# Kernel tuning notes

Measured on AMD Instinct MI355X. Metric: run time of the kernel, lower is better.

## Reference

```python
import jax, jax.numpy as jnp
import numpy as np

N = 100000      # nodes
E = 1600000     # edges (before self-loops)
F_IN = 128      # num_features
H = 4           # heads
C = 32          # out_channels per head (num_hidden)
SLOPE = 0.2     # leaky relu negative slope (alpha)


def setup_inputs() -> dict:
    key = jax.random.key(0)
    k = jax.random.split(key, 6)
    x = jax.random.normal(k[0], (N, F_IN), jnp.float32)
    edge_index = jax.random.randint(k[1], (2, E), 0, N, dtype=jnp.int64)
    W = jax.random.normal(k[2], (F_IN, H * C), jnp.float32) * (1.0 / np.sqrt(F_IN))
    att_src = jax.random.normal(k[3], (H, C), jnp.float32) * 0.1
    att_dst = jax.random.normal(k[4], (H, C), jnp.float32) * 0.1
    bias = jnp.zeros((H * C,), jnp.float32)
    return dict(x=x, W=W, att_src=att_src, att_dst=att_dst, bias=bias,
                edge_index=edge_index)


def reference(x, W, att_src, att_dst, bias, edge_index):
    # PyG GATConv (concat=True, add_self_loops=True), eval mode (dropout off).
    loops = jnp.arange(N, dtype=edge_index.dtype)
    ei = jnp.concatenate([edge_index, jnp.stack([loops, loops])], axis=1)
    src, dst = ei[0], ei[1]                     # [E+N]

    h = (x @ W).reshape(N, H, C)                # projected node features
    a_src = jnp.einsum('nhc,hc->nh', h, att_src)   # [N, H]
    a_dst = jnp.einsum('nhc,hc->nh', h, att_dst)   # [N, H]

    e = a_src[src] + a_dst[dst]                 # [E+N, H]
    e = jnp.where(e > 0, e, SLOPE * e)          # leaky relu

    # segment softmax over incoming edges of each dst node (per head)
    m = jax.lax.stop_gradient(jax.ops.segment_max(e, dst, num_segments=N))
    p = jnp.exp(e - m[dst])
    denom = jax.ops.segment_sum(p, dst, num_segments=N)
    alpha = p / (denom[dst] + 1e-16)            # [E+N, H]

    # weighted scatter-aggregate of source features
    out = jax.ops.segment_sum(alpha[:, :, None] * h[src], dst, num_segments=N)
    return out.reshape(N, H * C) + bias
```

## Files before the change

### kernel.cpp

```cpp
#include <hip/hip_runtime.h>
#include <hip/hip_bf16.h>
#include <math.h>

#define N_NODES 100000
#define F_IN    128
#define HC      128
#define NH      4
#define SLOPE   0.2f

#define PADK    136

#define NB      196
#define BSH     9
#define CAP     10240
#define CAPC    10752
#define CHUNK   2048
#define CURPAD  16

#define GEMM_BLOCKS 1563

typedef __attribute__((ext_vector_type(8))) short short8;
typedef __attribute__((ext_vector_type(4))) float f32x4;
typedef __attribute__((ext_vector_type(2))) float fx2;

static __device__ __forceinline__ float leaky(float x) { return x > 0.f ? x : SLOPE * x; }

static __device__ __forceinline__ short f2bs(float f) {
    __hip_bfloat16 b = __float2bfloat16(f);
    return *reinterpret_cast<short*>(&b);
}

__global__ __launch_bounds__(256) void k_pre(const float* __restrict__ W,
                                             unsigned short* __restrict__ wt,
                                             int* __restrict__ bucket_cursor)
{
    int t = blockIdx.x * 256 + threadIdx.x;
    if (t < 128 * 128) {
        int k = t >> 7, n = t & 127;
        wt[n * 128 + k] = (unsigned short)f2bs(W[k * HC + n]);
    }
    if (t < NB * CURPAD) bucket_cursor[t] = 0;
}

union SMem {
    struct {
        short xs[64 * PADK];
        short ws[128 * PADK];
    } g;
    struct {
        int ebuf[CHUNK];
        unsigned char bkt[CHUNK];
        int hist[256];
        int lexcl[257];
        int gbase[256];
        int sdata[256];
    } b;
};

__global__ __launch_bounds__(256) void k_main(const float* __restrict__ x,
                                              const unsigned short* __restrict__ wt,
                                              const float* __restrict__ att_src,
                                              const float* __restrict__ att_dst,
                                              unsigned short* __restrict__ hb,
                                              float* __restrict__ a_src,
                                              float* __restrict__ a_dst,
                                              const int* __restrict__ srcp,
                                              const int* __restrict__ dstp,
                                              int* __restrict__ bucket_cursor,
                                              int* __restrict__ eb, int E)
{
    __shared__ SMem sm;
    const int t = threadIdx.x;

    if (blockIdx.x < GEMM_BLOCKS) {
        const int r0 = blockIdx.x * 64;

        for (int i = t; i < 2048; i += 256) {
            int row = i >> 5, kq = (i & 31) * 4;
            int gr = r0 + row;
            float4 v = make_float4(0.f, 0.f, 0.f, 0.f);
            if (gr < N_NODES) v = ((const float4*)(x + (size_t)gr * F_IN))[i & 31];
            short* p = &sm.g.xs[row * PADK + kq];
            p[0] = f2bs(v.x); p[1] = f2bs(v.y); p[2] = f2bs(v.z); p[3] = f2bs(v.w);
        }
        for (int i = t; i < 2048; i += 256) {
            int n = i >> 4, k0 = (i & 15) * 8;
            *(float4*)&sm.g.ws[n * PADK + k0] = *(const float4*)&wt[n * 128 + k0];
        }
        __syncthreads();

        const int wave = t >> 6, lane = t & 63;
        const int quad = lane >> 4, l16 = lane & 15;
        const int wrow = wave * 16;

        f32x4 acc[8];
        #pragma unroll
        for (int nt = 0; nt < 8; ++nt) acc[nt] = (f32x4){0.f, 0.f, 0.f, 0.f};

        const short* ap = &sm.g.xs[(wrow + l16) * PADK + quad * 8];
        #pragma unroll
        for (int kb = 0; kb < 4; ++kb) {
            short8 a = *(const short8*)(ap + kb * 32);
            #pragma unroll
            for (int nt = 0; nt < 8; ++nt) {
                short8 b = *(const short8*)&sm.g.ws[(nt * 16 + l16) * PADK + kb * 32 + quad * 8];
                acc[nt] = __builtin_amdgcn_mfma_f32_16x16x32_bf16(a, b, acc[nt], 0, 0, 0);
            }
        }

        float att_s[8], att_d[8];
        #pragma unroll
        for (int nt = 0; nt < 8; ++nt) {
            att_s[nt] = att_src[nt * 16 + l16];
            att_d[nt] = att_dst[nt * 16 + l16];
        }

        #pragma unroll
        for (int g = 0; g < 4; ++g) {
            int r = r0 + wrow + quad * 4 + g;
            if (r < N_NODES) {
                #pragma unroll
                for (int nt = 0; nt < 8; ++nt)
                    hb[(size_t)r * HC + nt * 16 + l16] = (unsigned short)f2bs(acc[nt][g]);
            }
            float s0 = acc[0][g] * att_s[0] + acc[1][g] * att_s[1];
            float s1 = acc[2][g] * att_s[2] + acc[3][g] * att_s[3];
            float s2 = acc[4][g] * att_s[4] + acc[5][g] * att_s[5];
            float s3 = acc[6][g] * att_s[6] + acc[7][g] * att_s[7];
            float d0 = acc[0][g] * att_d[0] + acc[1][g] * att_d[1];
            float d1 = acc[2][g] * att_d[2] + acc[3][g] * att_d[3];
            float d2 = acc[4][g] * att_d[4] + acc[5][g] * att_d[5];
            float d3 = acc[6][g] * att_d[6] + acc[7][g] * att_d[7];
            #pragma unroll
            for (int o = 1; o < 16; o <<= 1) {
                s0 += __shfl_xor(s0, o); s1 += __shfl_xor(s1, o);
                s2 += __shfl_xor(s2, o); s3 += __shfl_xor(s3, o);
                d0 += __shfl_xor(d0, o); d1 += __shfl_xor(d1, o);
                d2 += __shfl_xor(d2, o); d3 += __shfl_xor(d3, o);
            }
            if (l16 == 0 && r < N_NODES) {
                *(float4*)&a_src[r * NH] = make_float4(s0, s1, s2, s3);
                *(float4*)&a_dst[r * NH] = make_float4(d0, d1, d2, d3);
            }
        }
    } else {
        const int base = (blockIdx.x - GEMM_BLOCKS) * CHUNK;

        sm.b.hist[t] = 0;
        __syncthreads();

        #pragma unroll
        for (int j = 0; j < CHUNK / 256; ++j) {
            int i = base + t + j * 256;
            if (i < E) atomicAdd(&sm.b.hist[dstp[i] >> BSH], 1);
        }
        __syncthreads();

        int cnt = sm.b.hist[t];
        sm.b.sdata[t] = cnt;
        __syncthreads();
        for (int o = 1; o < 256; o <<= 1) {
            int add = (t >= o) ? sm.b.sdata[t - o] : 0;
            __syncthreads();
            sm.b.sdata[t] += add;
            __syncthreads();
        }
        int excl = sm.b.sdata[t] - cnt;
        sm.b.lexcl[t] = excl;
        if (t == 255) sm.b.lexcl[256] = sm.b.sdata[255];
        sm.b.hist[t] = excl;
        int gb = 0;
        if (t < NB && cnt > 0) gb = atomicAdd(&bucket_cursor[t * CURPAD], cnt);
        sm.b.gbase[t] = t * CAP + gb;
        __syncthreads();

        #pragma unroll
        for (int j = 0; j < CHUNK / 256; ++j) {
            int i = base + t + j * 256;
            if (i < E) {
                int s = srcp[i], d = dstp[i];
                int b = d >> BSH;
                int r = atomicAdd(&sm.b.hist[b], 1);
                sm.b.ebuf[r] = (s << BSH) | (d & 511);
                sm.b.bkt[r] = (unsigned char)b;
            }
        }
        __syncthreads();

        const int blockTotal = sm.b.lexcl[256];
        for (int i = t; i < blockTotal; i += 256) {
            int b = sm.b.bkt[i];
            eb[sm.b.gbase[b] + (i - sm.b.lexcl[b])] = sm.b.ebuf[i];
        }
    }
}

__global__ __launch_bounds__(1024) void k_csr(const int* __restrict__ eb,
                                              const int* __restrict__ bucket_cursor,
                                              int* __restrict__ col,
                                              int2* __restrict__ rowse)
{
    __shared__ int deg[512];
    __shared__ int sdata[256];

    const int t  = threadIdx.x;
    const int b  = blockIdx.x;
    const int n0 = b * 512;
    const int cnt   = bucket_cursor[b * CURPAD];
    const int ebase = b * CAP;
    const int gofs  = b * CAPC;

    if (t < 512) deg[t] = (n0 + t < N_NODES) ? 1 : 0;
    __syncthreads();

    for (int i = t; i < cnt; i += 1024)
        atomicAdd(&deg[eb[ebase + i] & 511], 1);
    __syncthreads();

    int d0 = 0, d1 = 0, ps = 0;
    if (t < 256) {
        d0 = deg[2 * t]; d1 = deg[2 * t + 1];
        ps = d0 + d1;
        sdata[t] = ps;
    }
    __syncthreads();
    for (int o = 1; o < 256; o <<= 1) {
        int add = 0;
        if (t < 256 && t >= o) add = sdata[t - o];
        __syncthreads();
        if (t < 256) sdata[t] += add;
        __syncthreads();
    }
    if (t < 256) {
        int e0 = sdata[t] - ps;
        int e1 = e0 + d0;
        int na = n0 + 2 * t, nb2 = n0 + 2 * t + 1;
        if (na < N_NODES) {
            rowse[na] = make_int2(gofs + e0, gofs + e0 + d0);
            col[gofs + e0] = na;
        }
        if (nb2 < N_NODES) {
            rowse[nb2] = make_int2(gofs + e1, gofs + e1 + d1);
            col[gofs + e1] = nb2;
        }
        deg[2 * t]     = e0 + 1;
        deg[2 * t + 1] = e1 + 1;
    }
    __syncthreads();

    for (int i = t; i < cnt; i += 1024) {
        int v = eb[ebase + i];
        int r = atomicAdd(&deg[v & 511], 1);
        col[gofs + r] = v >> BSH;
    }
}

__global__ __launch_bounds__(256) void k_node(const unsigned short* __restrict__ hb,
                                              const float* __restrict__ a_src,
                                              const float* __restrict__ a_dst,
                                              const int2* __restrict__ rowse,
                                              const int* __restrict__ col,
                                              const float* __restrict__ bias,
                                              float* __restrict__ out)
{
    const int lane = threadIdx.x & 63;
    const int node = blockIdx.x * 4 + (threadIdx.x >> 6);
    if (node >= N_NODES) return;

    const int2 se = rowse[node];
    const int r0 = se.x, r1 = se.y;
    const int myh = lane >> 4;
    const float adm = a_dst[node * NH + myh];

    float denom = 0.f, acc0 = 0.f, acc1 = 0.f;
    int i = r0;
    for (; i + 8 <= r1; i += 8) {
        int s[8];
        #pragma unroll
        for (int j = 0; j < 8; ++j) s[j] = col[i + j];
        float as[8];
        #pragma unroll
        for (int j = 0; j < 8; ++j) as[j] = a_src[s[j] * NH + myh];
        unsigned int hv[8];
        #pragma unroll
        for (int j = 0; j < 8; ++j)
            hv[j] = *(const unsigned int*)&hb[(size_t)s[j] * HC + 2 * lane];
        #pragma unroll
        for (int j = 0; j < 8; ++j) {
            float p = __expf(leaky(as[j] + adm));
            denom += p;
            acc0 += p * __uint_as_float(hv[j] << 16);
            acc1 += p * __uint_as_float(hv[j] & 0xffff0000u);
        }
    }
    for (; i < r1; ++i) {
        int s = col[i];
        float p = __expf(leaky(a_src[s * NH + myh] + adm));
        unsigned int v = *(const unsigned int*)&hb[(size_t)s * HC + 2 * lane];
        denom += p;
        acc0 += p * __uint_as_float(v << 16);
        acc1 += p * __uint_as_float(v & 0xffff0000u);
    }

    float inv = 1.f / (denom + 1e-16f);
    fx2 o2;
    o2.x = acc0 * inv + bias[2 * lane];
    o2.y = acc1 * inv + bias[2 * lane + 1];
    __builtin_nontemporal_store(o2, (fx2*)&out[(size_t)node * HC + 2 * lane]);
}

extern "C" void kernel_launch(void* const* d_in, const int* in_sizes, int n_in,
                              void* d_out, int out_size, void* d_ws, size_t ws_size,
                              hipStream_t stream)
{
    const float* x       = (const float*)d_in[0];
    const float* W       = (const float*)d_in[1];
    const float* att_src = (const float*)d_in[2];
    const float* att_dst = (const float*)d_in[3];
    const float* bias    = (const float*)d_in[4];
    const int*   ei      = (const int*)d_in[5];
    const int E = in_sizes[5] / 2;
    const int* srcp = ei;
    const int* dstp = ei + E;
    float* out = (float*)d_out;

    char* wsb = (char*)d_ws;
    size_t off = 0;
    auto alloc = [&](size_t bytes) -> char* {
        char* p = wsb + off;
        off += (bytes + 255) & ~(size_t)255;
        return p;
    };
    unsigned short* hb = (unsigned short*)alloc((size_t)N_NODES * HC * sizeof(unsigned short));
    float* a_src   = (float*)alloc((size_t)N_NODES * NH * sizeof(float));
    float* a_dst   = (float*)alloc((size_t)N_NODES * NH * sizeof(float));
    int*   eb      = (int*)alloc((size_t)NB * CAP * sizeof(int));
    int*   col     = (int*)alloc((size_t)NB * CAPC * sizeof(int));
    int2*  rowse   = (int2*)alloc((size_t)N_NODES * sizeof(int2));
    int*   bcursor = (int*)alloc((size_t)NB * CURPAD * sizeof(int));
    unsigned short* wt = (unsigned short*)alloc(128 * 128 * sizeof(unsigned short));

    const int bucketBlocks = (E + CHUNK - 1) / CHUNK;

    k_pre<<<64, 256, 0, stream>>>(W, wt, bcursor);
    k_main<<<GEMM_BLOCKS + bucketBlocks, 256, 0, stream>>>(x, wt, att_src, att_dst,
                                                           hb, a_src, a_dst,
                                                           srcp, dstp, bcursor, eb, E);
    k_csr<<<NB, 1024, 0, stream>>>(eb, bcursor, col, rowse);
    k_node<<<(N_NODES + 3) / 4, 256, 0, stream>>>(hb, a_src, a_dst, rowse, col, bias, out);
}
```

Before: 251.0 us.

## Move bucketing to own kernel, fuse CSR build with GEMM, widen node gather

Edge bucketing now runs in its own kernel. The CSR construction (256-thread blocks) is merged into the same launch as the projection GEMM, so the CSR work overlaps with the dense compute and one launch goes away. The per-node aggregation is also restructured: each wave handles four edges at once with 16-byte feature loads per lane, then reduces across lane groups with shuffles before the store. The cost is an extra shuffle reduction, and the CSR part runs with fewer threads per bucket.

Result: no change. 247.4 us (-1.4%).

```diff
diff --git a/kernel.cpp b/kernel.cpp
--- a/kernel.cpp
+++ b/kernel.cpp
@@ -17,11 +17,8 @@
 #define CHUNK   2048
 #define CURPAD  16
 
-#define GEMM_BLOCKS 1563
-
 typedef __attribute__((ext_vector_type(8))) short short8;
 typedef __attribute__((ext_vector_type(4))) float f32x4;
-typedef __attribute__((ext_vector_type(2))) float fx2;
 
 static __device__ __forceinline__ float leaky(float x) { return x > 0.f ? x : SLOPE * x; }
 
@@ -40,6 +37,69 @@
         wt[n * 128 + k] = (unsigned short)f2bs(W[k * HC + n]);
     }
     if (t < NB * CURPAD) bucket_cursor[t] = 0;
+}
+
+__global__ __launch_bounds__(256) void k_bucket(const int* __restrict__ srcp,
+                                                const int* __restrict__ dstp,
+                                                int* __restrict__ bucket_cursor,
+                                                int* __restrict__ eb, int E)
+{
+    __shared__ int ebuf[CHUNK];
+    __shared__ unsigned char bkt[CHUNK];
+    __shared__ int hist[256];
+    __shared__ int lexcl[257];
+    __shared__ int gbase[256];
+    __shared__ int sdata[256];
+
+    const int t = threadIdx.x;
+    const int base = blockIdx.x * CHUNK;
+
+    hist[t] = 0;
+    __syncthreads();
+
+    #pragma unroll
+    for (int j = 0; j < CHUNK / 256; ++j) {
+        int i = base + t + j * 256;
+        if (i < E) atomicAdd(&hist[dstp[i] >> BSH], 1);
+    }
+    __syncthreads();
+
+    int cnt = hist[t];
+    sdata[t] = cnt;
+    __syncthreads();
+    for (int o = 1; o < 256; o <<= 1) {
+        int add = (t >= o) ? sdata[t - o] : 0;
+        __syncthreads();
+        sdata[t] += add;
+        __syncthreads();
+    }
+    int excl = sdata[t] - cnt;
+    lexcl[t] = excl;
+    if (t == 255) lexcl[256] = sdata[255];
+    hist[t] = excl;
+    int gb = 0;
+    if (t < NB && cnt > 0) gb = atomicAdd(&bucket_cursor[t * CURPAD], cnt);
+    gbase[t] = t * CAP + gb;
+    __syncthreads();
+
+    #pragma unroll
+    for (int j = 0; j < CHUNK / 256; ++j) {
+        int i = base + t + j * 256;
+        if (i < E) {
+            int s = srcp[i], d = dstp[i];
+            int b = d >> BSH;
+            int r = atomicAdd(&hist[b], 1);
+            ebuf[r] = (s << BSH) | (d & 511);
+            bkt[r] = (unsigned char)b;
+        }
+    }
+    __syncthreads();
+
+    const int blockTotal = lexcl[256];
+    for (int i = t; i < blockTotal; i += 256) {
+        int b = bkt[i];
+        eb[gbase[b] + (i - lexcl[b])] = ebuf[i];
+    }
 }
 
 union SMem {
@@ -48,32 +108,75 @@
         short ws[128 * PADK];
     } g;
     struct {
-        int ebuf[CHUNK];
-        unsigned char bkt[CHUNK];
-        int hist[256];
-        int lexcl[257];
-        int gbase[256];
+        int deg[512];
         int sdata[256];
-    } b;
+    } c;
 };
 
-__global__ __launch_bounds__(256) void k_main(const float* __restrict__ x,
-                                              const unsigned short* __restrict__ wt,
-                                              const float* __restrict__ att_src,
-                                              const float* __restrict__ att_dst,
-                                              unsigned short* __restrict__ hb,
-                                              float* __restrict__ a_src,
-                                              float* __restrict__ a_dst,
-                                              const int* __restrict__ srcp,
-                                              const int* __restrict__ dstp,
-                                              int* __restrict__ bucket_cursor,
-                                              int* __restrict__ eb, int E)
+__global__ __launch_bounds__(256) void k_fused(const float* __restrict__ x,
+                                               const unsigned short* __restrict__ wt,
+                                               const float* __restrict__ att_src,
+                                               const float* __restrict__ att_dst,
+                                               unsigned short* __restrict__ hb,
+                                               float* __restrict__ a_src,
+                                               float* __restrict__ a_dst,
+                                               const int* __restrict__ eb,
+                                               const int* __restrict__ bucket_cursor,
+                                               int* __restrict__ col,
+                                               int2* __restrict__ rowse)
 {
     __shared__ SMem sm;
     const int t = threadIdx.x;
 
-    if (blockIdx.x < GEMM_BLOCKS) {
-        const int r0 = blockIdx.x * 64;
+    if (blockIdx.x < NB) {
+        const int b  = blockIdx.x;
+        const int n0 = b * 512;
+        const int cnt   = bucket_cursor[b * CURPAD];
+        const int ebase = b * CAP;
+        const int gofs  = b * CAPC;
+
+        sm.c.deg[t]       = (n0 + t       < N_NODES) ? 1 : 0;
+        sm.c.deg[t + 256] = (n0 + t + 256 < N_NODES) ? 1 : 0;
+        __syncthreads();
+
+        for (int i = t; i < cnt; i += 256)
+            atomicAdd(&sm.c.deg[eb[ebase + i] & 511], 1);
+        __syncthreads();
+
+        int d0 = sm.c.deg[2 * t], d1 = sm.c.deg[2 * t + 1];
+        int ps = d0 + d1;
+        sm.c.sdata[t] = ps;
+        __syncthreads();
+        for (int o = 1; o < 256; o <<= 1) {
+            int add = (t >= o) ? sm.c.sdata[t - o] : 0;
+            __syncthreads();
+            sm.c.sdata[t] += add;
+            __syncthreads();
+        }
+        int e0 = sm.c.sdata[t] - ps;
+        int e1 = e0 + d0;
+        __syncthreads();
+
+        int na = n0 + 2 * t, nb2 = n0 + 2 * t + 1;
+        if (na < N_NODES) {
+            rowse[na] = make_int2(gofs + e0, gofs + e0 + d0);
+            col[gofs + e0] = na;
+        }
+        if (nb2 < N_NODES) {
+            rowse[nb2] = make_int2(gofs + e1, gofs + e1 + d1);
+            col[gofs + e1] = nb2;
+        }
+        sm.c.deg[2 * t]     = e0 + 1;
+        sm.c.deg[2 * t + 1] = e1 + 1;
+        __syncthreads();
+
+        for (int i = t; i < cnt; i += 256) {
+            int v = eb[ebase + i];
+            int r = atomicAdd(&sm.c.deg[v & 511], 1);
+            col[gofs + r] = v >> BSH;
+        }
+    } else {
+        const int r0 = (blockIdx.x - NB) * 64;
 
         for (int i = t; i < 2048; i += 256) {
             int row = i >> 5, kq = (i & 31) * 4;
@@ -143,115 +246,6 @@
                 *(float4*)&a_dst[r * NH] = make_float4(d0, d1, d2, d3);
             }
         }
-    } else {
-        const int base = (blockIdx.x - GEMM_BLOCKS) * CHUNK;
-
-        sm.b.hist[t] = 0;
-        __syncthreads();
-
-        #pragma unroll
-        for (int j = 0; j < CHUNK / 256; ++j) {
-            int i = base + t + j * 256;
-            if (i < E) atomicAdd(&sm.b.hist[dstp[i] >> BSH], 1);
-        }
-        __syncthreads();
-
-        int cnt = sm.b.hist[t];
-        sm.b.sdata[t] = cnt;
-        __syncthreads();
-        for (int o = 1; o < 256; o <<= 1) {
-            int add = (t >= o) ? sm.b.sdata[t - o] : 0;
-            __syncthreads();
-            sm.b.sdata[t] += add;
-            __syncthreads();
-        }
-        int excl = sm.b.sdata[t] - cnt;
-        sm.b.lexcl[t] = excl;
-        if (t == 255) sm.b.lexcl[256] = sm.b.sdata[255];
-        sm.b.hist[t] = excl;
-        int gb = 0;
-        if (t < NB && cnt > 0) gb = atomicAdd(&bucket_cursor[t * CURPAD], cnt);
-        sm.b.gbase[t] = t * CAP + gb;
-        __syncthreads();
-
-        #pragma unroll
-        for (int j = 0; j < CHUNK / 256; ++j) {
-            int i = base + t + j * 256;
-            if (i < E) {
-                int s = srcp[i], d = dstp[i];
-                int b = d >> BSH;
-                int r = atomicAdd(&sm.b.hist[b], 1);
-                sm.b.ebuf[r] = (s << BSH) | (d & 511);
-                sm.b.bkt[r] = (unsigned char)b;
-            }
-        }
-        __syncthreads();
-
-        const int blockTotal = sm.b.lexcl[256];
-        for (int i = t; i < blockTotal; i += 256) {
-            int b = sm.b.bkt[i];
-            eb[sm.b.gbase[b] + (i - sm.b.lexcl[b])] = sm.b.ebuf[i];
-        }
-    }
-}
-
-__global__ __launch_bounds__(1024) void k_csr(const int* __restrict__ eb,
-                                              const int* __restrict__ bucket_cursor,
-                                              int* __restrict__ col,
-                                              int2* __restrict__ rowse)
-{
-    __shared__ int deg[512];
-    __shared__ int sdata[256];
-
-    const int t  = threadIdx.x;
-    const int b  = blockIdx.x;
-    const int n0 = b * 512;
-    const int cnt   = bucket_cursor[b * CURPAD];
-    const int ebase = b * CAP;
-    const int gofs  = b * CAPC;
-
-    if (t < 512) deg[t] = (n0 + t < N_NODES) ? 1 : 0;
-    __syncthreads();
-
-    for (int i = t; i < cnt; i += 1024)
-        atomicAdd(&deg[eb[ebase + i] & 511], 1);
-    __syncthreads();
-
-    int d0 = 0, d1 = 0, ps = 0;
-    if (t < 256) {
-        d0 = deg[2 * t]; d1 = deg[2 * t + 1];
-        ps = d0 + d1;
-        sdata[t] = ps;
-    }
-    __syncthreads();
-    for (int o = 1; o < 256; o <<= 1) {
-        int add = 0;
-        if (t < 256 && t >= o) add = sdata[t - o];
-        __syncthreads();
-        if (t < 256) sdata[t] += add;
-        __syncthreads();
-    }
-    if (t < 256) {
-        int e0 = sdata[t] - ps;
-        int e1 = e0 + d0;
-        int na = n0 + 2 * t, nb2 = n0 + 2 * t + 1;
-        if (na < N_NODES) {
-            rowse[na] = make_int2(gofs + e0, gofs + e0 + d0);
-            col[gofs + e0] = na;
-        }
-        if (nb2 < N_NODES) {
-            rowse[nb2] = make_int2(gofs + e1, gofs + e1 + d1);
-            col[gofs + e1] = nb2;
-        }
-        deg[2 * t]     = e0 + 1;
-        deg[2 * t + 1] = e1 + 1;
-    }
-    __syncthreads();
-
-    for (int i = t; i < cnt; i += 1024) {
-        int v = eb[ebase + i];
-        int r = atomicAdd(&deg[v & 511], 1);
-        col[gofs + r] = v >> BSH;
     }
 }
 
@@ -267,46 +261,77 @@
     const int node = blockIdx.x * 4 + (threadIdx.x >> 6);
     if (node >= N_NODES) return;
 
+    const int g   = lane >> 4;
+    const int l16 = lane & 15;
+    const int myh = l16 >> 2;
+
     const int2 se = rowse[node];
-    const int r0 = se.x, r1 = se.y;
-    const int myh = lane >> 4;
+    const int r0 = se.x;
+    const int cnt = se.y - se.x;
+
     const float adm = a_dst[node * NH + myh];
 
-    float denom = 0.f, acc0 = 0.f, acc1 = 0.f;
-    int i = r0;
-    for (; i + 8 <= r1; i += 8) {
-        int s[8];
-        #pragma unroll
-        for (int j = 0; j < 8; ++j) s[j] = col[i + j];
-        float as[8];
-        #pragma unroll
-        for (int j = 0; j < 8; ++j) as[j] = a_src[s[j] * NH + myh];
-        unsigned int hv[8];
-        #pragma unroll
-        for (int j = 0; j < 8; ++j)
-            hv[j] = *(const unsigned int*)&hb[(size_t)s[j] * HC + 2 * lane];
-        #pragma unroll
-        for (int j = 0; j < 8; ++j) {
-            float p = __expf(leaky(as[j] + adm));
-            denom += p;
-            acc0 += p * __uint_as_float(hv[j] << 16);
-            acc1 += p * __uint_as_float(hv[j] & 0xffff0000u);
-        }
-    }
-    for (; i < r1; ++i) {
-        int s = col[i];
-        float p = __expf(leaky(a_src[s * NH + myh] + adm));
-        unsigned int v = *(const unsigned int*)&hb[(size_t)s * HC + 2 * lane];
+    float acc[8];
+    #pragma unroll
+    for (int k = 0; k < 8; ++k) acc[k] = 0.f;
+    float denom = 0.f;
+
+    int i = 0;
+    for (; i + 8 <= cnt; i += 8) {
+        int s0 = col[r0 + i + g];
+        int s1 = col[r0 + i + 4 + g];
+        float as0 = a_src[s0 * NH + myh];
+        float as1 = a_src[s1 * NH + myh];
+        uint4 h0 = ((const uint4*)(hb + (size_t)s0 * HC))[l16];
+        uint4 h1 = ((const uint4*)(hb + (size_t)s1 * HC))[l16];
+        float p0 = __expf(leaky(as0 + adm));
+        float p1 = __expf(leaky(as1 + adm));
+        denom += p0 + p1;
+        acc[0] += p0 * __uint_as_float(h0.x << 16)        + p1 * __uint_as_float(h1.x << 16);
+        acc[1] += p0 * __uint_as_float(h0.x & 0xffff0000u) + p1 * __uint_as_float(h1.x & 0xffff0000u);
+        acc[2] += p0 * __uint_as_float(h0.y << 16)        + p1 * __uint_as_float(h1.y << 16);
+        acc[3] += p0 * __uint_as_float(h0.y & 0xffff0000u) + p1 * __uint_as_float(h1.y & 0xffff0000u);
+        acc[4] += p0 * __uint_as_float(h0.z << 16)        + p1 * __uint_as_float(h1.z << 16);
+        acc[5] += p0 * __uint_as_float(h0.z & 0xffff0000u) + p1 * __uint_as_float(h1.z & 0xffff0000u);
+        acc[6] += p0 * __uint_as_float(h0.w << 16)        + p1 * __uint_as_float(h1.w << 16);
+        acc[7] += p0 * __uint_as_float(h0.w & 0xffff0000u) + p1 * __uint_as_float(h1.w & 0xffff0000u);
+    }
+    for (; i < cnt; i += 4) {
+        int e = i + g;
+        bool v = e < cnt;
+        int s = col[r0 + (v ? e : 0)];
+        float as = a_src[s * NH + myh];
+        uint4 h0 = ((const uint4*)(hb + (size_t)s * HC))[l16];
+        float p = v ? __expf(leaky(as + adm)) : 0.f;
         denom += p;
-        acc0 += p * __uint_as_float(v << 16);
-        acc1 += p * __uint_as_float(v & 0xffff0000u);
-    }
-
-    float inv = 1.f / (denom + 1e-16f);
-    fx2 o2;
-    o2.x = acc0 * inv + bias[2 * lane];
-    o2.y = acc1 * inv + bias[2 * lane + 1];
-    __builtin_nontemporal_store(o2, (fx2*)&out[(size_t)node * HC + 2 * lane]);
+        acc[0] += p * __uint_as_float(h0.x << 16);
+        acc[1] += p * __uint_as_float(h0.x & 0xffff0000u);
+        acc[2] += p * __uint_as_float(h0.y << 16);
+        acc[3] += p * __uint_as_float(h0.y & 0xffff0000u);
+        acc[4] += p * __uint_as_float(h0.z << 16);
+        acc[5] += p * __uint_as_float(h0.z & 0xffff0000u);
+        acc[6] += p * __uint_as_float(h0.w << 16);
+        acc[7] += p * __uint_as_float(h0.w & 0xffff0000u);
+    }
+
+    #pragma unroll
+    for (int o = 16; o < 64; o <<= 1) {
+        denom += __shfl_xor(denom, o);
+        #pragma unroll
+        for (int k = 0; k < 8; ++k) acc[k] += __shfl_xor(acc[k], o);
+    }
+
+    if (g == 0) {
+        float inv = 1.f / (denom + 1e-16f);
+        const float* bp = &bias[l16 * 8];
+        f32x4 o0, o1;
+        o0.x = acc[0] * inv + bp[0]; o0.y = acc[1] * inv + bp[1];
+        o0.z = acc[2] * inv + bp[2]; o0.w = acc[3] * inv + bp[3];
+        o1.x = acc[4] * inv + bp[4]; o1.y = acc[5] * inv + bp[5];
+        o1.z = acc[6] * inv + bp[6]; o1.w = acc[7] * inv + bp[7];
+        __builtin_nontemporal_store(o0, (f32x4*)&out[(size_t)node * HC + l16 * 8]);
+        __builtin_nontemporal_store(o1, (f32x4*)&out[(size_t)node * HC + l16 * 8 + 4]);
+    }
 }
 
 extern "C" void kernel_launch(void* const* d_in, const int* in_sizes, int n_in,
@@ -341,11 +366,12 @@
     unsigned short* wt = (unsigned short*)alloc(128 * 128 * sizeof(unsigned short));
 
     const int bucketBlocks = (E + CHUNK - 1) / CHUNK;
+    const int gemmBlocks   = (N_NODES + 63) / 64;
 
     k_pre<<<64, 256, 0, stream>>>(W, wt, bcursor);
-    k_main<<<GEMM_BLOCKS + bucketBlocks, 256, 0, stream>>>(x, wt, att_src, att_dst,
-                                                           hb, a_src, a_dst,
-                                                           srcp, dstp, bcursor, eb, E);
-    k_csr<<<NB, 1024, 0, stream>>>(eb, bcursor, col, rowse);
+    k_bucket<<<bucketBlocks, 256, 0, stream>>>(srcp, dstp, bcursor, eb, E);
+    k_fused<<<NB + gemmBlocks, 256, 0, stream>>>(x, wt, att_src, att_dst,
+                                                 hb, a_src, a_dst,
+                                                 eb, bcursor, col, rowse);
     k_node<<<(N_NODES + 3) / 4, 256, 0, stream>>>(hb, a_src, a_dst, rowse, col, bias, out);
 }
```

## Split wave into 4 edge groups with 16B gathers and software-pipelined prefetch

Applied to the files above, without the earlier changes.

The node aggregation kernel now assigns each wave's four 16-lane groups to different edges. Each lane gathers 8 bf16 features with a 16-byte load, and the loop prefetches the next edges' column indices, attention scores and feature rows one iteration ahead. Partial sums are then combined with cross-group shuffles. Separately, the fused GEMM/bucketing kernel now schedules bucket blocks first and keeps src/dst in registers instead of reloading them. This trades more registers and a final reduction for more memory-level parallelism and fewer, wider gather requests.

Result: faster. 245.1 us (-2.4%).

```diff
diff --git a/kernel.cpp b/kernel.cpp
--- a/kernel.cpp
+++ b/kernel.cpp
@@ -17,11 +17,8 @@
 #define CHUNK   2048
 #define CURPAD  16
 
-#define GEMM_BLOCKS 1563
-
 typedef __attribute__((ext_vector_type(8))) short short8;
 typedef __attribute__((ext_vector_type(4))) float f32x4;
-typedef __attribute__((ext_vector_type(2))) float fx2;
 
 static __device__ __forceinline__ float leaky(float x) { return x > 0.f ? x : SLOPE * x; }
 
@@ -67,13 +64,65 @@
                                               const int* __restrict__ srcp,
                                               const int* __restrict__ dstp,
                                               int* __restrict__ bucket_cursor,
-                                              int* __restrict__ eb, int E)
+                                              int* __restrict__ eb, int E,
+                                              int bucketBlocks)
 {
     __shared__ SMem sm;
     const int t = threadIdx.x;
 
-    if (blockIdx.x < GEMM_BLOCKS) {
-        const int r0 = blockIdx.x * 64;
+    if ((int)blockIdx.x < bucketBlocks) {
+        const int base = blockIdx.x * CHUNK;
+
+        sm.b.hist[t] = 0;
+        __syncthreads();
+
+        int sreg[8], dreg[8];
+        #pragma unroll
+        for (int j = 0; j < CHUNK / 256; ++j) {
+            int i = base + t + j * 256;
+            bool v = i < E;
+            sreg[j] = v ? srcp[i] : 0;
+            dreg[j] = v ? dstp[i] : -1;
+            if (v) atomicAdd(&sm.b.hist[dreg[j] >> BSH], 1);
+        }
+        __syncthreads();
+
+        int cnt = sm.b.hist[t];
+        sm.b.sdata[t] = cnt;
+        __syncthreads();
+        for (int o = 1; o < 256; o <<= 1) {
+            int add = (t >= o) ? sm.b.sdata[t - o] : 0;
+            __syncthreads();
+            sm.b.sdata[t] += add;
+            __syncthreads();
+        }
+        int excl = sm.b.sdata[t] - cnt;
+        sm.b.lexcl[t] = excl;
+        if (t == 255) sm.b.lexcl[256] = sm.b.sdata[255];
+        sm.b.hist[t] = excl;
+        int gb = 0;
+        if (t < NB && cnt > 0) gb = atomicAdd(&bucket_cursor[t * CURPAD], cnt);
+        sm.b.gbase[t] = t * CAP + gb;
+        __syncthreads();
+
+        #pragma unroll
+        for (int j = 0; j < CHUNK / 256; ++j) {
+            if (dreg[j] >= 0) {
+                int b = dreg[j] >> BSH;
+                int r = atomicAdd(&sm.b.hist[b], 1);
+                sm.b.ebuf[r] = (sreg[j] << BSH) | (dreg[j] & 511);
+                sm.b.bkt[r] = (unsigned char)b;
+            }
+        }
+        __syncthreads();
+
+        const int blockTotal = sm.b.lexcl[256];
+        for (int i = t; i < blockTotal; i += 256) {
+            int b = sm.b.bkt[i];
+            eb[sm.b.gbase[b] + (i - sm.b.lexcl[b])] = sm.b.ebuf[i];
+        }
+    } else {
+        const int r0 = (blockIdx.x - bucketBlocks) * 64;
 
         for (int i = t; i < 2048; i += 256) {
             int row = i >> 5, kq = (i & 31) * 4;
@@ -143,55 +192,6 @@
                 *(float4*)&a_dst[r * NH] = make_float4(d0, d1, d2, d3);
             }
         }
-    } else {
-        const int base = (blockIdx.x - GEMM_BLOCKS) * CHUNK;
-
-        sm.b.hist[t] = 0;
-        __syncthreads();
-
-        #pragma unroll
-        for (int j = 0; j < CHUNK / 256; ++j) {
-            int i = base + t + j * 256;
-            if (i < E) atomicAdd(&sm.b.hist[dstp[i] >> BSH], 1);
-        }
-        __syncthreads();
-
-        int cnt = sm.b.hist[t];
-        sm.b.sdata[t] = cnt;
-        __syncthreads();
-        for (int o = 1; o < 256; o <<= 1) {
-            int add = (t >= o) ? sm.b.sdata[t - o] : 0;
-            __syncthreads();
-            sm.b.sdata[t] += add;
-            __syncthreads();
-        }
-        int excl = sm.b.sdata[t] - cnt;
-        sm.b.lexcl[t] = excl;
-        if (t == 255) sm.b.lexcl[256] = sm.b.sdata[255];
-        sm.b.hist[t] = excl;
-        int gb = 0;
-        if (t < NB && cnt > 0) gb = atomicAdd(&bucket_cursor[t * CURPAD], cnt);
-        sm.b.gbase[t] = t * CAP + gb;
-        __syncthreads();
-
-        #pragma unroll
-        for (int j = 0; j < CHUNK / 256; ++j) {
-            int i = base + t + j * 256;
-            if (i < E) {
-                int s = srcp[i], d = dstp[i];
-                int b = d >> BSH;
-                int r = atomicAdd(&sm.b.hist[b], 1);
-                sm.b.ebuf[r] = (s << BSH) | (d & 511);
-                sm.b.bkt[r] = (unsigned char)b;
-            }
-        }
-        __syncthreads();
-
-        const int blockTotal = sm.b.lexcl[256];
-        for (int i = t; i < blockTotal; i += 256) {
-            int b = sm.b.bkt[i];
-            eb[sm.b.gbase[b] + (i - sm.b.lexcl[b])] = sm.b.ebuf[i];
-        }
     }
 }
 
@@ -267,46 +267,95 @@
     const int node = blockIdx.x * 4 + (threadIdx.x >> 6);
     if (node >= N_NODES) return;
 
+    const int g   = lane >> 4;
+    const int l16 = lane & 15;
+    const int myh = l16 >> 2;
+
     const int2 se = rowse[node];
-    const int r0 = se.x, r1 = se.y;
-    const int myh = lane >> 4;
+    const int r0 = se.x;
+    const int cnt = se.y - se.x;
+
     const float adm = a_dst[node * NH + myh];
 
-    float denom = 0.f, acc0 = 0.f, acc1 = 0.f;
-    int i = r0;
-    for (; i + 8 <= r1; i += 8) {
-        int s[8];
-        #pragma unroll
-        for (int j = 0; j < 8; ++j) s[j] = col[i + j];
-        float as[8];
-        #pragma unroll
-        for (int j = 0; j < 8; ++j) as[j] = a_src[s[j] * NH + myh];
-        unsigned int hv[8];
-        #pragma unroll
-        for (int j = 0; j < 8; ++j)
-            hv[j] = *(const unsigned int*)&hb[(size_t)s[j] * HC + 2 * lane];
-        #pragma unroll
-        for (int j = 0; j < 8; ++j) {
-            float p = __expf(leaky(as[j] + adm));
-            denom += p;
-            acc0 += p * __uint_as_float(hv[j] << 16);
-            acc1 += p * __uint_as_float(hv[j] & 0xffff0000u);
-        }
-    }
-    for (; i < r1; ++i) {
-        int s = col[i];
-        float p = __expf(leaky(a_src[s * NH + myh] + adm));
-        unsigned int v = *(const unsigned int*)&hb[(size_t)s * HC + 2 * lane];
-        denom += p;
-        acc0 += p * __uint_as_float(v << 16);
-        acc1 += p * __uint_as_float(v & 0xffff0000u);
-    }
-
-    float inv = 1.f / (denom + 1e-16f);
-    fx2 o2;
-    o2.x = acc0 * inv + bias[2 * lane];
-    o2.y = acc1 * inv + bias[2 * lane + 1];
-    __builtin_nontemporal_store(o2, (fx2*)&out[(size_t)node * HC + 2 * lane]);
+    float acc[8];
+    #pragma unroll
+    for (int k = 0; k < 8; ++k) acc[k] = 0.f;
+    float denom = 0.f;
+
+    bool vA0, vA1, vB0, vB1;
+    int  cB0, cB1;
+    float aA0, aA1;
+    uint4 hA0, hA1;
+
+    {
+        int e0 = g, e1 = 4 + g;
+        vA0 = e0 < cnt; vA1 = e1 < cnt;
+        int c0 = col[r0 + (vA0 ? e0 : 0)];
+        int c1 = col[r0 + (vA1 ? e1 : 0)];
+        aA0 = a_src[c0 * NH + myh];
+        aA1 = a_src[c1 * NH + myh];
+        hA0 = ((const uint4*)(hb + (size_t)c0 * HC))[l16];
+        hA1 = ((const uint4*)(hb + (size_t)c1 * HC))[l16];
+    }
+    {
+        int e0 = 8 + g, e1 = 12 + g;
+        vB0 = e0 < cnt; vB1 = e1 < cnt;
+        cB0 = col[r0 + (vB0 ? e0 : 0)];
+        cB1 = col[r0 + (vB1 ? e1 : 0)];
+    }
+
+    for (int i = 0; i < cnt; i += 8) {
+        const bool more = (i + 8 < cnt);
+        float aN0 = 0.f, aN1 = 0.f;
+        uint4 hN0 = make_uint4(0, 0, 0, 0), hN1 = make_uint4(0, 0, 0, 0);
+        int cC0 = 0, cC1 = 0;
+        bool vC0 = false, vC1 = false;
+        if (more) {
+            aN0 = a_src[cB0 * NH + myh];
+            aN1 = a_src[cB1 * NH + myh];
+            hN0 = ((const uint4*)(hb + (size_t)cB0 * HC))[l16];
+            hN1 = ((const uint4*)(hb + (size_t)cB1 * HC))[l16];
+            int e0 = i + 16 + g, e1 = i + 20 + g;
+            vC0 = e0 < cnt; vC1 = e1 < cnt;
+            cC0 = col[r0 + (vC0 ? e0 : 0)];
+            cC1 = col[r0 + (vC1 ? e1 : 0)];
+        }
+        float p0 = vA0 ? __expf(leaky(aA0 + adm)) : 0.f;
+        float p1 = vA1 ? __expf(leaky(aA1 + adm)) : 0.f;
+        denom += p0 + p1;
+        acc[0] += p0 * __uint_as_float(hA0.x << 16)         + p1 * __uint_as_float(hA1.x << 16);
+        acc[1] += p0 * __uint_as_float(hA0.x & 0xffff0000u) + p1 * __uint_as_float(hA1.x & 0xffff0000u);
+        acc[2] += p0 * __uint_as_float(hA0.y << 16)         + p1 * __uint_as_float(hA1.y << 16);
+        acc[3] += p0 * __uint_as_float(hA0.y & 0xffff0000u) + p1 * __uint_as_float(hA1.y & 0xffff0000u);
+        acc[4] += p0 * __uint_as_float(hA0.z << 16)         + p1 * __uint_as_float(hA1.z << 16);
+        acc[5] += p0 * __uint_as_float(hA0.z & 0xffff0000u) + p1 * __uint_as_float(hA1.z & 0xffff0000u);
+        acc[6] += p0 * __uint_as_float(hA0.w << 16)         + p1 * __uint_as_float(hA1.w << 16);
+        acc[7] += p0 * __uint_as_float(hA0.w & 0xffff0000u) + p1 * __uint_as_float(hA1.w & 0xffff0000u);
+        if (more) {
+            vA0 = vB0; vA1 = vB1;
+            aA0 = aN0; aA1 = aN1; hA0 = hN0; hA1 = hN1;
+            vB0 = vC0; vB1 = vC1; cB0 = cC0; cB1 = cC1;
+        }
+    }
+
+    #pragma unroll
+    for (int o = 16; o < 64; o <<= 1) {
+        denom += __shfl_xor(denom, o);
+        #pragma unroll
+        for (int k = 0; k < 8; ++k) acc[k] += __shfl_xor(acc[k], o);
+    }
+
+    if (g == 0) {
+        float inv = 1.f / (denom + 1e-16f);
+        const float* bp = &bias[l16 * 8];
+        f32x4 o0, o1;
+        o0.x = acc[0] * inv + bp[0]; o0.y = acc[1] * inv + bp[1];
+        o0.z = acc[2] * inv + bp[2]; o0.w = acc[3] * inv + bp[3];
+        o1.x = acc[4] * inv + bp[4]; o1.y = acc[5] * inv + bp[5];
+        o1.z = acc[6] * inv + bp[6]; o1.w = acc[7] * inv + bp[7];
+        __builtin_nontemporal_store(o0, (f32x4*)&out[(size_t)node * HC + l16 * 8]);
+        __builtin_nontemporal_store(o1, (f32x4*)&out[(size_t)node * HC + l16 * 8 + 4]);
+    }
 }
 
 extern "C" void kernel_launch(void* const* d_in, const int* in_sizes, int n_in,
@@ -341,11 +390,13 @@
     unsigned short* wt = (unsigned short*)alloc(128 * 128 * sizeof(unsigned short));
 
     const int bucketBlocks = (E + CHUNK - 1) / CHUNK;
+    const int gemmBlocks   = (N_NODES + 63) / 64;
 
     k_pre<<<64, 256, 0, stream>>>(W, wt, bcursor);
-    k_main<<<GEMM_BLOCKS + bucketBlocks, 256, 0, stream>>>(x, wt, att_src, att_dst,
-                                                           hb, a_src, a_dst,
-                                                           srcp, dstp, bcursor, eb, E);
+    k_main<<<bucketBlocks + gemmBlocks, 256, 0, stream>>>(x, wt, att_src, att_dst,
+                                                          hb, a_src, a_dst,
+                                                          srcp, dstp, bcursor, eb, E,
+                                                          bucketBlocks);
     k_csr<<<NB, 1024, 0, stream>>>(eb, bcursor, col, rowse);
     k_node<<<(N_NODES + 3) / 4, 256, 0, stream>>>(hb, a_src, a_dst, rowse, col, bias, out);
 }
```
